# Optimization experiments

Hardware: AMD Instinct MI355X
Metric: run time of the kernel (lower is better)

Reference implementation:

```python
import jax, jax.numpy as jnp
import numpy as np

AVG_LEN = 60.0
EPS = 1e-5
L, B, C, E = 48, 16, 128, 128
N_AGG = 15  # 5 + 10 * len(['sum'])


def setup_inputs() -> dict:
    key = jax.random.key(0)
    k0, k1, k2, k3 = jax.random.split(key, 4)
    T = jax.random.normal(k0, (L, L, B, C), jnp.float32)
    mask = jax.random.randint(k1, (L, L, B), 0, 2) > 0
    running_mean = jnp.zeros((C,), jnp.float32)
    running_var = jnp.ones((C,), jnp.float32)
    bn_weight = jnp.ones((C,), jnp.float32)
    bn_bias = jnp.zeros((C,), jnp.float32)
    w1 = jax.random.normal(k2, (C, E), jnp.float32) / np.sqrt(C).astype(np.float32)
    b1 = jnp.zeros((E,), jnp.float32)
    w2 = jax.random.normal(k3, (N_AGG * E, C), jnp.float32) / np.sqrt(N_AGG * E).astype(np.float32)
    b2 = jnp.zeros((C,), jnp.float32)
    return dict(T=T, mask=mask, running_mean=running_mean, running_var=running_var,
                bn_weight=bn_weight, bn_bias=bn_bias, w1=w1, b1=b1, w2=w2, b2=b2)


def reference(T, mask, running_mean, running_var, bn_weight, bn_bias, w1, b1, w2, b2):
    n = T.shape[0]
    # MaskedBatchNorm2d, eval mode (running stats)
    Tn = (T - running_mean) / jnp.sqrt(running_var + EPS) * bn_weight + bn_bias
    H = jax.nn.silu(Tn @ w1 + b1)                      # [L, L, B, E]
    eye = jnp.eye(n, dtype=bool)                       # [L, L]
    mf = mask[..., None].astype(H.dtype)               # [L, L, B, 1]
    mdf = (mask & eye[:, :, None])[..., None].astype(H.dtype)
    idx = jnp.arange(n)
    diag = H[idx, idx]                                 # [L, B, E]

    def dembed(x):  # [L, B, E] -> [L, L, B, E] with x on the (0,1)-diagonal
        return jnp.where(eye[:, :, None, None], x[:, None], jnp.zeros((), H.dtype))

    bc = lambda x: jnp.broadcast_to(x, H.shape)
    Hm = H * mf
    row_agg = jnp.sum(Hm, axis=0) / AVG_LEN            # [L, B, E]
    col_agg = jnp.sum(Hm, axis=1) / AVG_LEN            # [L, B, E]
    diag_agg = jnp.sum(H * mdf, axis=(0, 1)) / AVG_LEN # [B, E]
    all_agg = jnp.sum(Hm, axis=(0, 1)) / (AVG_LEN ** 2)  # [B, E]

    parts = [
        dembed(diag), bc(diag[None]), bc(diag[:, None]), jnp.swapaxes(H, 0, 1), H,
        dembed(row_agg), dembed(col_agg),
        dembed(jnp.broadcast_to(diag_agg[None], diag.shape)),
        bc(diag_agg[None, None]), bc(row_agg[None]), bc(col_agg[None]),
        bc(all_agg[None, None]), bc(col_agg[:, None]), bc(row_agg[:, None]),
        bc(all_agg[None, None]),
    ]
    outputs = jnp.concatenate(parts, axis=3)           # [L, L, B, 15*E]
    return outputs @ w2 + b2
```

## Files before the change

### kernel.cpp

```cpp
#include <hip/hip_runtime.h>

typedef __attribute__((ext_vector_type(8))) short short8;
typedef __attribute__((ext_vector_type(4))) float f32x4;
typedef __attribute__((ext_vector_type(4))) unsigned short ushort4_t;

#define NL 48
#define NB 16
#define NROWS (NL*NL*NB)

#define HB_N     (NROWS*128/2)
#define HB_OFF   0
#define W34T_OFF (HB_OFF + HB_N)
#define WD_OFF   (W34T_OFF + 16384)
#define X2_OFF   (WD_OFF + 73728)
#define VEC_N    (NL*NB*128)
#define RA_OFF   (X2_OFF + 147456)
#define AJ_OFF   (RA_OFF + VEC_N)
#define AI_OFF   (AJ_OFF + VEC_N)
#define AD_OFF   (AI_OFF + VEC_N)
#define AB_OFF   (AD_OFF + VEC_N)
#define DGA_OFF  (AB_OFF + NB*128)
#define FLAG_OFF (DGA_OFF + NB*128)

__device__ __forceinline__ float silu_f(float x) { return x / (1.0f + __expf(-x)); }
__device__ __forceinline__ unsigned short f2bf(float x) {
  union { float f; unsigned u; } v; v.f = x;
  unsigned r = v.u + 0x7fffu + ((v.u >> 16) & 1u);
  return (unsigned short)(r >> 16);
}
__device__ __forceinline__ float bf2f(unsigned short h) {
  union { unsigned u; float f; } v; v.u = ((unsigned)h) << 16; return v.f;
}
__device__ __forceinline__ void gload_lds16(const void* g, void* l) {
  __builtin_amdgcn_global_load_lds(
      (const __attribute__((address_space(1))) unsigned*)g,
      (__attribute__((address_space(3))) unsigned*)l, 16, 0, 0);
}

__global__ __launch_bounds__(256) void kA(const float* __restrict__ T,
    const float* __restrict__ rmean, const float* __restrict__ rvar,
    const float* __restrict__ bw, const float* __restrict__ bb,
    const float* __restrict__ w1, const float* __restrict__ b1,
    const float* __restrict__ w2, const unsigned char* __restrict__ mb,
    unsigned short* __restrict__ Hb, unsigned short* __restrict__ w34t,
    unsigned short* __restrict__ wd, int* __restrict__ flag)
{
  __shared__ __align__(16) char SM[49152];
  __shared__ int any;
  char* XDS = SM;
  char* WDS = SM + 16384;
  float* tt = (float*)SM;
  int tid = threadIdx.x;
  int blk = blockIdx.x;

  if (blk >= 576) {
    int pb = blk - 576;
    if (pb < 8) {
      int k0 = (pb & 3)*64, n0 = (pb >> 2)*64;
      #pragma unroll
      for (int it = 0; it < 16; ++it) { int f = it*256+tid; int kk=f>>6, nn=f&63;
        int k = k0+kk; int slice = (k < 128) ? 4 : 3;
        tt[kk*65+nn] = w2[slice*16384 + (k&127)*128 + n0+nn]; }
      __syncthreads();
      #pragma unroll
      for (int it = 0; it < 16; ++it) { int f = it*256+tid; int nn=f>>6, kk=f&63;
        w34t[(n0+nn)*256 + k0+kk] = f2bf(tt[kk*65+nn]); }
    } else if (pb < 44) {
      int q = pb-8; int k0 = (q%6)*64, n0 = (q/6)*64;
      int nq = n0 >> 7, kq = k0 >> 7;
      int slice;
      {
        const int sl_aj[3] = {1,9,10};
        const int sl_ai[3] = {2,13,12};
        const int sl_ad[3] = {0,5,6};
        slice = (nq==0) ? sl_aj[kq] : (nq==1) ? sl_ai[kq] : sl_ad[kq];
      }
      int nb = n0 & 127;
      #pragma unroll
      for (int it = 0; it < 16; ++it) { int f = it*256+tid; int kk=f>>6, nn=f&63;
        tt[kk*65+nn] = w2[slice*16384 + ((k0&127)+kk)*128 + nb+nn]; }
      __syncthreads();
      #pragma unroll
      for (int it = 0; it < 16; ++it) { int f = it*256+tid; int nn=f>>6, kk=f&63;
        wd[(n0+nn)*384 + k0+kk] = f2bf(tt[kk*65+nn]); }
    } else {
      if (tid == 0) any = 0;
      __syncthreads();
      int acc = 0;
      #pragma unroll
      for (int k2 = 0; k2 < 12; ++k2) {
        uchar4 v = ((const uchar4*)mb)[tid + k2*256];
        acc |= v.y | v.z | v.w;
      }
      if (acc) atomicOr(&any, 1);
      __syncthreads();
      if (tid == 0) *flag = any ? 1 : 4;
    }
    return;
  }

  int m0 = blk * 64;
  int cbase = (tid & 31) * 4;
  float scr[4], shr[4];
  #pragma unroll
  for (int u = 0; u < 4; ++u) {
    float s = bw[cbase+u] * rsqrtf(rvar[cbase+u] + 1e-5f);
    scr[u] = s; shr[u] = bb[cbase+u] - rmean[cbase+u] * s;
  }
  #pragma unroll
  for (int t = 0; t < 8; ++t) {
    int f = t*256 + tid;
    int r = f >> 5, c4 = f & 31;
    f32x4 v = __builtin_nontemporal_load((const f32x4*)&T[(m0 + r)*128 + c4*4]);
    ushort4_t p;
    p.x = f2bf(v.x*scr[0] + shr[0]); p.y = f2bf(v.y*scr[1] + shr[1]);
    p.z = f2bf(v.z*scr[2] + shr[2]); p.w = f2bf(v.w*scr[3] + shr[3]);
    *(ushort4_t*)(XDS + r*256 + ((c4*8) ^ ((r & 7) << 4))) = p;
  }
  {
    int n = tid & 127, ch = (tid >> 7) * 8;
    #pragma unroll
    for (int cc = 0; cc < 8; ++cc) {
      int c = ch + cc;
      short8 v;
      #pragma unroll
      for (int j = 0; j < 8; ++j)
        ((unsigned short*)&v)[j] = f2bf(w1[(c*8 + j)*128 + n]);
      *(short8*)(WDS + n*256 + ((c*16) ^ ((n & 7) << 4))) = v;
    }
  }
  __syncthreads();

  int wave = tid >> 6, lane = tid & 63;
  int ln = lane & 15, lg = lane >> 4;
  int rw = (wave >> 1) * 32, cw = (wave & 1) * 64;
  int swz = (ln & 7) << 4;
  f32x4 acc[2][4];
  #pragma unroll
  for (int mt = 0; mt < 2; ++mt)
    #pragma unroll
    for (int nt = 0; nt < 4; ++nt) acc[mt][nt] = (f32x4){0.f,0.f,0.f,0.f};

  #pragma unroll
  for (int ks = 0; ks < 4; ++ks) {
    int kb = ks*64 + lg*16;
    short8 a[2], b[4];
    #pragma unroll
    for (int mt = 0; mt < 2; ++mt)
      a[mt] = *(const short8*)(XDS + (rw + mt*16 + ln)*256 + (kb ^ swz));
    #pragma unroll
    for (int nt = 0; nt < 4; ++nt)
      b[nt] = *(const short8*)(WDS + (cw + nt*16 + ln)*256 + (kb ^ swz));
    #pragma unroll
    for (int mt = 0; mt < 2; ++mt)
      #pragma unroll
      for (int nt = 0; nt < 4; ++nt)
        acc[mt][nt] = __builtin_amdgcn_mfma_f32_16x16x32_bf16(a[mt], b[nt], acc[mt][nt], 0, 0, 0);
  }
  float b1v[4];
  #pragma unroll
  for (int nt = 0; nt < 4; ++nt) b1v[nt] = b1[cw + nt*16 + ln];
  #pragma unroll
  for (int mt = 0; mt < 2; ++mt)
    #pragma unroll
    for (int q = 0; q < 4; ++q) {
      int m = m0 + rw + mt*16 + 4*lg + q;
      #pragma unroll
      for (int nt = 0; nt < 4; ++nt) {
        float x = acc[mt][nt][q] + b1v[nt];
        Hb[m*128 + cw + nt*16 + ln] = f2bf(silu_f(x));
      }
    }
}

__global__ __launch_bounds__(128) void kAgg(const unsigned short* __restrict__ Hb,
    const unsigned char* __restrict__ mb, const int* __restrict__ flag,
    float* __restrict__ ra, unsigned short* __restrict__ X2)
{
  int p = blockIdx.x, b = blockIdx.y;
  int tid = threadIdx.x;
  int s = *flag;
  int half = tid >> 6;
  int t = tid & 63;
  float a0 = 0.f, a1 = 0.f;
  #pragma unroll 16
  for (int q = 0; q < NL; ++q) {
    int mi = half ? ((q*NL + p)*NB + b) : ((p*NL + q)*NB + b);
    float mv = (float)mb[mi*s];
    unsigned u = *(const unsigned*)(Hb + mi*128 + 2*t);
    a0 += mv * bf2f((unsigned short)(u & 0xffffu));
    a1 += mv * bf2f((unsigned short)(u >> 16));
  }
  a0 *= (1.0f/60.0f); a1 *= (1.0f/60.0f);
  int ix = p*NB + b;
  unsigned pk = ((unsigned)f2bf(a1) << 16) | (unsigned)f2bf(a0);
  if (half) {
    *(float2*)(ra + ix*128 + 2*t) = make_float2(a0, a1);
    *(unsigned*)(X2 + ix*384 + 128 + 2*t) = pk;
  } else {
    *(unsigned*)(X2 + ix*384 + 256 + 2*t) = pk;
    unsigned d = *(const unsigned*)(Hb + ((p*NL + p)*NB + b)*128 + 2*t);
    *(unsigned*)(X2 + ix*384 + 2*t) = d;
  }
}

__global__ __launch_bounds__(256) void kDm(const unsigned short* __restrict__ X2,
    const unsigned short* __restrict__ wd,
    const unsigned short* __restrict__ Hb, const unsigned char* __restrict__ mb,
    const int* __restrict__ flag, const float* __restrict__ ra,
    const float* __restrict__ w2, const float* __restrict__ b2,
    float* __restrict__ Aj, float* __restrict__ Ai, float* __restrict__ Adg,
    float* __restrict__ Ab, float* __restrict__ Dga)
{
  int tid = threadIdx.x;
  if (blockIdx.y == 3) {
    int b = blockIdx.x;
    __shared__ float aas[128], dgs[128];
    int e = tid & 127;
    if (tid < 128) {
      int s = *flag;
      float aa = 0.f, dg = 0.f;
      #pragma unroll 8
      for (int p = 0; p < NL; ++p) {
        aa += ra[(p*NB + b)*128 + e];
        int mi = (p*NL + p)*NB + b;
        dg += (float)mb[mi*s] * bf2f(Hb[mi*128 + e]);
      }
      aas[e] = aa * (1.0f/60.0f);
      dgs[e] = dg * (1.0f/60.0f);
    }
    __syncthreads();
    if (tid < 128) {
      float ab = b2[e];
      #pragma unroll 8
      for (int k = 0; k < 128; ++k) {
        int o = k*128 + e;
        ab += dgs[k]*w2[8*16384 + o] + aas[k]*(w2[11*16384 + o] + w2[14*16384 + o]);
      }
      Ab[b*128 + e] = ab;
    } else {
      float dga = 0.f;
      #pragma unroll 8
      for (int k = 0; k < 128; ++k)
        dga += dgs[k]*w2[7*16384 + k*128 + e];
      Dga[b*128 + e] = dga;
    }
    return;
  }
  if (blockIdx.x >= 12) return;

  __shared__ __align__(16) char ADS[64*256];
  __shared__ __align__(16) char BDS[128*256];
  int m0 = blockIdx.x * 64;
  int n0 = blockIdx.y * 128;

  int wave = tid >> 6, lane = tid & 63;
  int ln = lane & 15, lg = lane >> 4;
  int rw = (wave >> 1) * 32, cw = (wave & 1) * 64;
  int swzk = (ln & 7) << 4;
  f32x4 acc[2][4];
  #pragma unroll
  for (int mt = 0; mt < 2; ++mt)
    #pragma unroll
    for (int nt = 0; nt < 4; ++nt) acc[mt][nt] = (f32x4){0.f,0.f,0.f,0.f};

  for (int kc = 0; kc < 3; ++kc) {
    if (kc) __syncthreads();
    #pragma unroll
    for (int t = 0; t < 4; ++t) {
      int f = t*256 + tid;
      int r = f >> 4, c16 = f & 15;
      const char* gp = (const char*)X2 + (m0 + r)*768 + kc*256 + ((c16 ^ (r & 7))*16);
      gload_lds16(gp, ADS + (f & ~63)*16);
    }
    #pragma unroll
    for (int t = 0; t < 8; ++t) {
      int f = t*256 + tid;
      int r = f >> 4, c16 = f & 15;
      const char* gp = (const char*)wd + (n0 + r)*768 + kc*256 + ((c16 ^ (r & 7))*16);
      gload_lds16(gp, BDS + (f & ~63)*16);
    }
    __syncthreads();
    #pragma unroll
    for (int ks = 0; ks < 4; ++ks) {
      int kb = ks*64 + lg*16;
      short8 a[2], b[4];
      #pragma unroll
      for (int mt = 0; mt < 2; ++mt)
        a[mt] = *(const short8*)(ADS + (rw + mt*16 + ln)*256 + (kb ^ swzk));
      #pragma unroll
      for (int nt = 0; nt < 4; ++nt)
        b[nt] = *(const short8*)(BDS + (cw + nt*16 + ln)*256 + (kb ^ swzk));
      #pragma unroll
      for (int mt = 0; mt < 2; ++mt)
        #pragma unroll
        for (int nt = 0; nt < 4; ++nt)
          acc[mt][nt] = __builtin_amdgcn_mfma_f32_16x16x32_bf16(a[mt], b[nt], acc[mt][nt], 0, 0, 0);
    }
  }
  float* outp = (blockIdx.y == 0) ? Aj : (blockIdx.y == 1) ? Ai : Adg;
  #pragma unroll
  for (int mt = 0; mt < 2; ++mt)
    #pragma unroll
    for (int q = 0; q < 4; ++q) {
      int row = m0 + rw + mt*16 + 4*lg + q;
      #pragma unroll
      for (int nt = 0; nt < 4; ++nt)
        outp[row*128 + cw + nt*16 + ln] = acc[mt][nt][q];
    }
}

__global__ __launch_bounds__(256) void kE(const unsigned short* __restrict__ Hb,
    const unsigned short* __restrict__ w34t,
    const float* __restrict__ Aj, const float* __restrict__ Ai,
    const float* __restrict__ Adg, const float* __restrict__ Ab,
    const float* __restrict__ Dga,
    float* __restrict__ out)
{
  __shared__ __align__(16) char ADS[64*256];
  __shared__ __align__(16) char BDS[128*256];
  int tid = threadIdx.x;
  int bi = blockIdx.x / 12;
  int j0 = (blockIdx.x % 12) * 4;
  int m0 = (bi*NL + j0) * NB;

  int wave = tid >> 6, lane = tid & 63;
  int ln = lane & 15, lg = lane >> 4;
  int rw = (wave >> 1) * 32, cw = (wave & 1) * 64;
  int swz = (ln & 7) << 4;
  f32x4 acc[2][4];
  #pragma unroll
  for (int mt = 0; mt < 2; ++mt)
    #pragma unroll
    for (int nt = 0; nt < 4; ++nt) acc[mt][nt] = (f32x4){0.f,0.f,0.f,0.f};

  #pragma unroll
  for (int half = 0; half < 2; ++half) {
    if (half) __syncthreads();
    #pragma unroll
    for (int t = 0; t < 4; ++t) {
      int f = t*256 + tid;
      int r = f >> 4, c16 = f & 15;
      int srcrow = (half == 0) ? (m0 + r) : (((j0 + (r >> 4))*NL + bi)*NB + (r & 15));
      const char* gp = (const char*)Hb + (size_t)srcrow*256 + ((c16 ^ (r & 7))*16);
      gload_lds16(gp, ADS + (f & ~63)*16);
    }
    #pragma unroll
    for (int t = 0; t < 8; ++t) {
      int f = t*256 + tid;
      int r = f >> 4, c16 = f & 15;
      const char* gp = (const char*)w34t + r*512 + half*256 + ((c16 ^ (r & 7))*16);
      gload_lds16(gp, BDS + (f & ~63)*16);
    }
    __syncthreads();
    #pragma unroll
    for (int ks = 0; ks < 4; ++ks) {
      int kb = ks*64 + lg*16;
      short8 a[2], b[4];
      #pragma unroll
      for (int mt = 0; mt < 2; ++mt)
        a[mt] = *(const short8*)(ADS + (rw + mt*16 + ln)*256 + (kb ^ swz));
      #pragma unroll
      for (int nt = 0; nt < 4; ++nt)
        b[nt] = *(const short8*)(BDS + (cw + nt*16 + ln)*256 + (kb ^ swz));
      #pragma unroll
      for (int mt = 0; mt < 2; ++mt)
        #pragma unroll
        for (int nt = 0; nt < 4; ++nt)
          acc[mt][nt] = __builtin_amdgcn_mfma_f32_16x16x32_bf16(a[mt], b[nt], acc[mt][nt], 0, 0, 0);
    }
  }

  #pragma unroll
  for (int mt = 0; mt < 2; ++mt) {
    int tb = rw + mt*16;
    int jj = tb >> 4;
    int j = j0 + jj;
    bool isdiag = (bi == j);
    #pragma unroll
    for (int q = 0; q < 4; ++q) {
      int b = 4*lg + q;
      int m = (bi*NL + j)*NB + b;
      #pragma unroll
      for (int nt = 0; nt < 4; ++nt) {
        int n = cw + nt*16 + ln;
        float add = Aj[(j*NB + b)*128 + n] + Ai[(bi*NB + b)*128 + n] + Ab[b*128 + n];
        if (isdiag) add += Adg[(bi*NB + b)*128 + n] + Dga[b*128 + n];
        __builtin_nontemporal_store(acc[mt][nt][q] + add, &out[m*128 + n]);
      }
    }
  }
}

extern "C" void kernel_launch(void* const* d_in, const int* in_sizes, int n_in,
                              void* d_out, int out_size, void* d_ws, size_t ws_size,
                              hipStream_t stream) {
  (void)in_sizes; (void)n_in; (void)out_size; (void)ws_size;
  const float* T      = (const float*)d_in[0];
  const unsigned char* mask = (const unsigned char*)d_in[1];
  const float* rmean  = (const float*)d_in[2];
  const float* rvar   = (const float*)d_in[3];
  const float* bw     = (const float*)d_in[4];
  const float* bb     = (const float*)d_in[5];
  const float* w1     = (const float*)d_in[6];
  const float* b1     = (const float*)d_in[7];
  const float* w2     = (const float*)d_in[8];
  const float* b2     = (const float*)d_in[9];
  float* ws  = (float*)d_ws;
  float* out = (float*)d_out;

  unsigned short* Hb   = (unsigned short*)(ws + HB_OFF);
  unsigned short* w34t = (unsigned short*)(ws + W34T_OFF);
  unsigned short* wd   = (unsigned short*)(ws + WD_OFF);
  unsigned short* X2   = (unsigned short*)(ws + X2_OFF);
  float* ra   = ws + RA_OFF;
  float* Aj   = ws + AJ_OFF;
  float* Ai   = ws + AI_OFF;
  float* Adg  = ws + AD_OFF;
  float* Ab   = ws + AB_OFF;
  float* Dga  = ws + DGA_OFF;
  int*   flag = (int*)(ws + FLAG_OFF);

  kA<<<621, 256, 0, stream>>>(T, rmean, rvar, bw, bb, w1, b1, w2, mask,
                              Hb, w34t, wd, flag);
  kAgg<<<dim3(NL, NB), 128, 0, stream>>>(Hb, mask, flag, ra, X2);
  kDm<<<dim3(16, 4), 256, 0, stream>>>(X2, wd, Hb, mask, flag, ra, w2, b2,
                                       Aj, Ai, Adg, Ab, Dga);
  kE<<<NROWS/64, 256, 0, stream>>>(Hb, w34t, Aj, Ai, Adg, Ab, Dga, out);
}
```

Baseline: 52.53 us.

## Fuse aggregation, dense and output kernels into one persistent kernel with grid barriers

Replaces the kAgg, kDm and kE launches with a single persistent kernel of 512 blocks. The stages are separated by software grid barriers built on an atomic counter, which kA resets. The goal is to remove launch overhead and inter-kernel gaps. In exchange, the barriers spin-wait and assume all 512 blocks are co-resident (launch bounds 256,3), and the output GEMM now loops over two tiles per block. The nontemporal output store is also replaced with a plain store.

```diff
diff --git a/kernel.cpp b/kernel.cpp
--- a/kernel.cpp
+++ b/kernel.cpp
@@ -21,6 +21,7 @@
 #define AB_OFF   (AD_OFF + VEC_N)
 #define DGA_OFF  (AB_OFF + NB*128)
 #define FLAG_OFF (DGA_OFF + NB*128)
+#define CNT_OFF  (FLAG_OFF + 1)
 
 __device__ __forceinline__ float silu_f(float x) { return x / (1.0f + __expf(-x)); }
 __device__ __forceinline__ unsigned short f2bf(float x) {
@@ -35,6 +36,17 @@
   __builtin_amdgcn_global_load_lds(
       (const __attribute__((address_space(1))) unsigned*)g,
       (__attribute__((address_space(3))) unsigned*)l, 16, 0, 0);
+}
+__device__ __forceinline__ void gridbar(int* cnt, int target) {
+  __syncthreads();
+  if (threadIdx.x == 0) {
+    __threadfence();
+    __hip_atomic_fetch_add(cnt, 1, __ATOMIC_RELEASE, __HIP_MEMORY_SCOPE_AGENT);
+    while (__hip_atomic_load(cnt, __ATOMIC_ACQUIRE, __HIP_MEMORY_SCOPE_AGENT) < target)
+      __builtin_amdgcn_s_sleep(1);
+    __threadfence();
+  }
+  __syncthreads();
 }
 
 __global__ __launch_bounds__(256) void kA(const float* __restrict__ T,
@@ -43,7 +55,7 @@
     const float* __restrict__ w1, const float* __restrict__ b1,
     const float* __restrict__ w2, const unsigned char* __restrict__ mb,
     unsigned short* __restrict__ Hb, unsigned short* __restrict__ w34t,
-    unsigned short* __restrict__ wd, int* __restrict__ flag)
+    unsigned short* __restrict__ wd, int* __restrict__ flag, int* __restrict__ cnt)
 {
   __shared__ __align__(16) char SM[49152];
   __shared__ int any;
@@ -94,7 +106,7 @@
       }
       if (acc) atomicOr(&any, 1);
       __syncthreads();
-      if (tid == 0) *flag = any ? 1 : 4;
+      if (tid == 0) { *flag = any ? 1 : 4; cnt[0] = 0; }
     }
     return;
   }
@@ -173,15 +185,15 @@
     }
 }
 
-__global__ __launch_bounds__(128) void kAgg(const unsigned short* __restrict__ Hb,
-    const unsigned char* __restrict__ mb, const int* __restrict__ flag,
-    float* __restrict__ ra, unsigned short* __restrict__ X2)
+#define MGRID 512
+
+__device__ __forceinline__ void agg_task(const unsigned short* __restrict__ Hb,
+    const unsigned char* __restrict__ mb, int s,
+    float* __restrict__ ra, unsigned short* __restrict__ X2, int task, int st)
 {
-  int p = blockIdx.x, b = blockIdx.y;
-  int tid = threadIdx.x;
-  int s = *flag;
-  int half = tid >> 6;
-  int t = tid & 63;
+  int p = task >> 4, b = task & 15;
+  int half = st >> 6;
+  int t = st & 63;
   float a0 = 0.f, a1 = 0.f;
   #pragma unroll 16
   for (int q = 0; q < NL; ++q) {
@@ -204,21 +216,89 @@
   }
 }
 
-__global__ __launch_bounds__(256) void kDm(const unsigned short* __restrict__ X2,
-    const unsigned short* __restrict__ wd,
+__global__ __launch_bounds__(256, 3) void kMega(
     const unsigned short* __restrict__ Hb, const unsigned char* __restrict__ mb,
-    const int* __restrict__ flag, const float* __restrict__ ra,
+    const int* __restrict__ flag, float* __restrict__ ra,
+    unsigned short* __restrict__ X2, const unsigned short* __restrict__ wd,
+    const unsigned short* __restrict__ w34t,
     const float* __restrict__ w2, const float* __restrict__ b2,
     float* __restrict__ Aj, float* __restrict__ Ai, float* __restrict__ Adg,
-    float* __restrict__ Ab, float* __restrict__ Dga)
+    float* __restrict__ Ab, float* __restrict__ Dga,
+    float* __restrict__ out, int* __restrict__ cnt)
 {
+  __shared__ __align__(16) char ADS[64*256];
+  __shared__ __align__(16) char BDS[128*256];
   int tid = threadIdx.x;
-  if (blockIdx.y == 3) {
-    int b = blockIdx.x;
-    __shared__ float aas[128], dgs[128];
+  int bid = blockIdx.x;
+  int wave = tid >> 6, lane = tid & 63;
+  int ln = lane & 15, lg = lane >> 4;
+  int rw = (wave >> 1) * 32, cw = (wave & 1) * 64;
+  int swz = (ln & 7) << 4;
+  int s = *flag;
+
+  if (tid < 128) agg_task(Hb, mb, s, ra, X2, bid, tid);
+  else if (bid < 256) agg_task(Hb, mb, s, ra, X2, MGRID + bid, tid - 128);
+
+  gridbar(cnt, MGRID);
+
+  if (bid < 36) {
+    int m0 = (bid % 12) * 64;
+    int n0 = (bid / 12) * 128;
+    f32x4 acc[2][4];
+    #pragma unroll
+    for (int mt = 0; mt < 2; ++mt)
+      #pragma unroll
+      for (int nt = 0; nt < 4; ++nt) acc[mt][nt] = (f32x4){0.f,0.f,0.f,0.f};
+    for (int kc = 0; kc < 3; ++kc) {
+      if (kc) __syncthreads();
+      #pragma unroll
+      for (int t = 0; t < 4; ++t) {
+        int f = t*256 + tid;
+        int r = f >> 4, c16 = f & 15;
+        const char* gp = (const char*)X2 + (m0 + r)*768 + kc*256 + ((c16 ^ (r & 7))*16);
+        gload_lds16(gp, ADS + (f & ~63)*16);
+      }
+      #pragma unroll
+      for (int t = 0; t < 8; ++t) {
+        int f = t*256 + tid;
+        int r = f >> 4, c16 = f & 15;
+        const char* gp = (const char*)wd + (n0 + r)*768 + kc*256 + ((c16 ^ (r & 7))*16);
+        gload_lds16(gp, BDS + (f & ~63)*16);
+      }
+      __syncthreads();
+      #pragma unroll
+      for (int ks = 0; ks < 4; ++ks) {
+        int kb = ks*64 + lg*16;
+        short8 a[2], b[4];
+        #pragma unroll
+        for (int mt = 0; mt < 2; ++mt)
+          a[mt] = *(const short8*)(ADS + (rw + mt*16 + ln)*256 + (kb ^ swz));
+        #pragma unroll
+        for (int nt = 0; nt < 4; ++nt)
+          b[nt] = *(const short8*)(BDS + (cw + nt*16 + ln)*256 + (kb ^ swz));
+        #pragma unroll
+        for (int mt = 0; mt < 2; ++mt)
+          #pragma unroll
+          for (int nt = 0; nt < 4; ++nt)
+            acc[mt][nt] = __builtin_amdgcn_mfma_f32_16x16x32_bf16(a[mt], b[nt], acc[mt][nt], 0, 0, 0);
+      }
+    }
+    float* outp = (n0 == 0) ? Aj : (n0 == 128) ? Ai : Adg;
+    #pragma unroll
+    for (int mt = 0; mt < 2; ++mt)
+      #pragma unroll
+      for (int q = 0; q < 4; ++q) {
+        int row = m0 + rw + mt*16 + 4*lg + q;
+        #pragma unroll
+        for (int nt = 0; nt < 4; ++nt)
+          outp[row*128 + cw + nt*16 + ln] = acc[mt][nt][q];
+      }
+  } else if (bid < 52) {
+    int b = bid - 36;
+    float* aas = (float*)ADS;
+    float* dgs = (float*)(ADS + 512);
     int e = tid & 127;
     if (tid < 128) {
-      int s = *flag;
       float aa = 0.f, dg = 0.f;
       #pragma unroll 8
       for (int p = 0; p < NL; ++p) {
@@ -245,148 +325,76 @@
         dga += dgs[k]*w2[7*16384 + k*128 + e];
       Dga[b*128 + e] = dga;
     }
-    return;
-  }
-  if (blockIdx.x >= 12) return;
-
-  __shared__ __align__(16) char ADS[64*256];
-  __shared__ __align__(16) char BDS[128*256];
-  int m0 = blockIdx.x * 64;
-  int n0 = blockIdx.y * 128;
-
-  int wave = tid >> 6, lane = tid & 63;
-  int ln = lane & 15, lg = lane >> 4;
-  int rw = (wave >> 1) * 32, cw = (wave & 1) * 64;
-  int swzk = (ln & 7) << 4;
-  f32x4 acc[2][4];
-  #pragma unroll
-  for (int mt = 0; mt < 2; ++mt)
-    #pragma unroll
-    for (int nt = 0; nt < 4; ++nt) acc[mt][nt] = (f32x4){0.f,0.f,0.f,0.f};
-
-  for (int kc = 0; kc < 3; ++kc) {
-    if (kc) __syncthreads();
-    #pragma unroll
-    for (int t = 0; t < 4; ++t) {
-      int f = t*256 + tid;
-      int r = f >> 4, c16 = f & 15;
-      const char* gp = (const char*)X2 + (m0 + r)*768 + kc*256 + ((c16 ^ (r & 7))*16);
-      gload_lds16(gp, ADS + (f & ~63)*16);
-    }
-    #pragma unroll
-    for (int t = 0; t < 8; ++t) {
-      int f = t*256 + tid;
-      int r = f >> 4, c16 = f & 15;
-      const char* gp = (const char*)wd + (n0 + r)*768 + kc*256 + ((c16 ^ (r & 7))*16);
-      gload_lds16(gp, BDS + (f & ~63)*16);
-    }
+  }
+
+  gridbar(cnt, 2*MGRID);
+
+  #pragma unroll 1
+  for (int rep = 0; rep < 2; ++rep) {
+    int t = bid + rep*MGRID;
+    if (t >= 576) break;
+    int bi = t / 12;
+    int j0 = (t % 12) * 4;
+    int m0 = (bi*NL + j0) * NB;
     __syncthreads();
-    #pragma unroll
-    for (int ks = 0; ks < 4; ++ks) {
-      int kb = ks*64 + lg*16;
-      short8 a[2], b[4];
-      #pragma unroll
-      for (int mt = 0; mt < 2; ++mt)
-        a[mt] = *(const short8*)(ADS + (rw + mt*16 + ln)*256 + (kb ^ swzk));
-      #pragma unroll
-      for (int nt = 0; nt < 4; ++nt)
-        b[nt] = *(const short8*)(BDS + (cw + nt*16 + ln)*256 + (kb ^ swzk));
-      #pragma unroll
-      for (int mt = 0; mt < 2; ++mt)
+    f32x4 acc[2][4];
+    #pragma unroll
+    for (int mt = 0; mt < 2; ++mt)
+      #pragma unroll
+      for (int nt = 0; nt < 4; ++nt) acc[mt][nt] = (f32x4){0.f,0.f,0.f,0.f};
+    #pragma unroll
+    for (int half = 0; half < 2; ++half) {
+      if (half) __syncthreads();
+      #pragma unroll
+      for (int tt = 0; tt < 4; ++tt) {
+        int f = tt*256 + tid;
+        int r = f >> 4, c16 = f & 15;
+        int srcrow = (half == 0) ? (m0 + r) : (((j0 + (r >> 4))*NL + bi)*NB + (r & 15));
+        const char* gp = (const char*)Hb + (size_t)srcrow*256 + ((c16 ^ (r & 7))*16);
+        gload_lds16(gp, ADS + (f & ~63)*16);
+      }
+      #pragma unroll
+      for (int tt = 0; tt < 8; ++tt) {
+        int f = tt*256 + tid;
+        int r = f >> 4, c16 = f & 15;
+        const char* gp = (const char*)w34t + r*512 + half*256 + ((c16 ^ (r & 7))*16);
+        gload_lds16(gp, BDS + (f & ~63)*16);
+      }
+      __syncthreads();
+      #pragma unroll
+      for (int ks = 0; ks < 4; ++ks) {
+        int kb = ks*64 + lg*16;
+        short8 a[2], b[4];
+        #pragma unroll
+        for (int mt = 0; mt < 2; ++mt)
+          a[mt] = *(const short8*)(ADS + (rw + mt*16 + ln)*256 + (kb ^ swz));
         #pragma unroll
         for (int nt = 0; nt < 4; ++nt)
-          acc[mt][nt] = __builtin_amdgcn_mfma_f32_16x16x32_bf16(a[mt], b[nt], acc[mt][nt], 0, 0, 0);
-    }
-  }
-  float* outp = (blockIdx.y == 0) ? Aj : (blockIdx.y == 1) ? Ai : Adg;
-  #pragma unroll
-  for (int mt = 0; mt < 2; ++mt)
-    #pragma unroll
-    for (int q = 0; q < 4; ++q) {
-      int row = m0 + rw + mt*16 + 4*lg + q;
-      #pragma unroll
-      for (int nt = 0; nt < 4; ++nt)
-        outp[row*128 + cw + nt*16 + ln] = acc[mt][nt][q];
-    }
-}
-
-__global__ __launch_bounds__(256) void kE(const unsigned short* __restrict__ Hb,
-    const unsigned short* __restrict__ w34t,
-    const float* __restrict__ Aj, const float* __restrict__ Ai,
-    const float* __restrict__ Adg, const float* __restrict__ Ab,
-    const float* __restrict__ Dga,
-    float* __restrict__ out)
-{
-  __shared__ __align__(16) char ADS[64*256];
-  __shared__ __align__(16) char BDS[128*256];
-  int tid = threadIdx.x;
-  int bi = blockIdx.x / 12;
-  int j0 = (blockIdx.x % 12) * 4;
-  int m0 = (bi*NL + j0) * NB;
-
-  int wave = tid >> 6, lane = tid & 63;
-  int ln = lane & 15, lg = lane >> 4;
-  int rw = (wave >> 1) * 32, cw = (wave & 1) * 64;
-  int swz = (ln & 7) << 4;
-  f32x4 acc[2][4];
-  #pragma unroll
-  for (int mt = 0; mt < 2; ++mt)
-    #pragma unroll
-    for (int nt = 0; nt < 4; ++nt) acc[mt][nt] = (f32x4){0.f,0.f,0.f,0.f};
-
-  #pragma unroll
-  for (int half = 0; half < 2; ++half) {
-    if (half) __syncthreads();
-    #pragma unroll
-    for (int t = 0; t < 4; ++t) {
-      int f = t*256 + tid;
-      int r = f >> 4, c16 = f & 15;
-      int srcrow = (half == 0) ? (m0 + r) : (((j0 + (r >> 4))*NL + bi)*NB + (r & 15));
-      const char* gp = (const char*)Hb + (size_t)srcrow*256 + ((c16 ^ (r & 7))*16);
-      gload_lds16(gp, ADS + (f & ~63)*16);
-    }
-    #pragma unroll
-    for (int t = 0; t < 8; ++t) {
-      int f = t*256 + tid;
-      int r = f >> 4, c16 = f & 15;
-      const char* gp = (const char*)w34t + r*512 + half*256 + ((c16 ^ (r & 7))*16);
-      gload_lds16(gp, BDS + (f & ~63)*16);
-    }
-    __syncthreads();
-    #pragma unroll
-    for (int ks = 0; ks < 4; ++ks) {
-      int kb = ks*64 + lg*16;
-      short8 a[2], b[4];
-      #pragma unroll
-      for (int mt = 0; mt < 2; ++mt)
-        a[mt] = *(const short8*)(ADS + (rw + mt*16 + ln)*256 + (kb ^ swz));
-      #pragma unroll
-      for (int nt = 0; nt < 4; ++nt)
-        b[nt] = *(const short8*)(BDS + (cw + nt*16 + ln)*256 + (kb ^ swz));
-      #pragma unroll
-      for (int mt = 0; mt < 2; ++mt)
-        #pragma unroll
-        for (int nt = 0; nt < 4; ++nt)
-          acc[mt][nt] = __builtin_amdgcn_mfma_f32_16x16x32_bf16(a[mt], b[nt], acc[mt][nt], 0, 0, 0);
-    }
-  }
-
-  #pragma unroll
-  for (int mt = 0; mt < 2; ++mt) {
-    int tb = rw + mt*16;
-    int jj = tb >> 4;
-    int j = j0 + jj;
-    bool isdiag = (bi == j);
-    #pragma unroll
-    for (int q = 0; q < 4; ++q) {
-      int b = 4*lg + q;
-      int m = (bi*NL + j)*NB + b;
-      #pragma unroll
-      for (int nt = 0; nt < 4; ++nt) {
-        int n = cw + nt*16 + ln;
-        float add = Aj[(j*NB + b)*128 + n] + Ai[(bi*NB + b)*128 + n] + Ab[b*128 + n];
-        if (isdiag) add += Adg[(bi*NB + b)*128 + n] + Dga[b*128 + n];
-        __builtin_nontemporal_store(acc[mt][nt][q] + add, &out[m*128 + n]);
+          b[nt] = *(const short8*)(BDS + (cw + nt*16 + ln)*256 + (kb ^ swz));
+        #pragma unroll
+        for (int mt = 0; mt < 2; ++mt)
+          #pragma unroll
+          for (int nt = 0; nt < 4; ++nt)
+            acc[mt][nt] = __builtin_amdgcn_mfma_f32_16x16x32_bf16(a[mt], b[nt], acc[mt][nt], 0, 0, 0);
+      }
+    }
+    #pragma unroll
+    for (int mt = 0; mt < 2; ++mt) {
+      int tb = rw + mt*16;
+      int jj = tb >> 4;
+      int j = j0 + jj;
+      bool isdiag = (bi == j);
+      #pragma unroll
+      for (int q = 0; q < 4; ++q) {
+        int b = 4*lg + q;
+        int m = (bi*NL + j)*NB + b;
+        #pragma unroll
+        for (int nt = 0; nt < 4; ++nt) {
+          int n = cw + nt*16 + ln;
+          float add = Aj[(j*NB + b)*128 + n] + Ai[(bi*NB + b)*128 + n] + Ab[b*128 + n];
+          if (isdiag) add += Adg[(bi*NB + b)*128 + n] + Dga[b*128 + n];
+          out[m*128 + n] = acc[mt][nt][q] + add;
+        }
       }
     }
   }
@@ -420,11 +428,10 @@
   float* Ab   = ws + AB_OFF;
   float* Dga  = ws + DGA_OFF;
   int*   flag = (int*)(ws + FLAG_OFF);
+  int*   cnt  = (int*)(ws + CNT_OFF);
 
   kA<<<621, 256, 0, stream>>>(T, rmean, rvar, bw, bb, w1, b1, w2, mask,
-                              Hb, w34t, wd, flag);
-  kAgg<<<dim3(NL, NB), 128, 0, stream>>>(Hb, mask, flag, ra, X2);
-  kDm<<<dim3(16, 4), 256, 0, stream>>>(X2, wd, Hb, mask, flag, ra, w2, b2,
-                                       Aj, Ai, Adg, Ab, Dga);
-  kE<<<NROWS/64, 256, 0, stream>>>(Hb, w34t, Aj, Ai, Adg, Ab, Dga, out);
-}
+                              Hb, w34t, wd, flag, cnt);
+  kMega<<<MGRID, 256, 0, stream>>>(Hb, mask, flag, ra, X2, wd, w34t, w2, b2,
+                                   Aj, Ai, Adg, Ab, Dga, out, cnt);
+}
```

After: 199.9 us. +280.5%, slower.
